# Optimization experiments

Measured on AMD Instinct MI355X. Metric: run time of the kernel, lower is better.

The kernel has to match this reference:

```python
import jax, jax.numpy as jnp
import numpy as np

DIM_Q = 512
DIM_K = 512
DIM_V = 512
NUM_HEADS = 8
B, NQ, NK = 8, 1024, 1024
EPS = 1e-5


def _layer_norm(x, gamma, beta):
    mu = jnp.mean(x, axis=-1, keepdims=True)
    var = jnp.var(x, axis=-1, keepdims=True)
    return (x - mu) * jax.lax.rsqrt(var + EPS) * gamma + beta


def setup_inputs() -> dict:
    key = jax.random.key(0)
    ks = jax.random.split(key, 12)

    def lin(k, fan_in, fan_out):
        bound = 1.0 / np.sqrt(fan_in)
        kw, kb = jax.random.split(k)
        W = jax.random.uniform(kw, (fan_in, fan_out), jnp.float32, -bound, bound)
        b = jax.random.uniform(kb, (fan_out,), jnp.float32, -bound, bound)
        return W, b

    Q = jax.random.normal(ks[0], (B, NQ, DIM_Q), jnp.float32)
    K = jax.random.normal(ks[1], (B, NK, DIM_K), jnp.float32)
    Wq, bq = lin(ks[2], DIM_Q, DIM_V)
    Wk, bk = lin(ks[3], DIM_K, DIM_V)
    Wv, bv = lin(ks[4], DIM_K, DIM_V)
    Wo, bo = lin(ks[5], DIM_V, DIM_V)
    g0 = jnp.ones((DIM_V,), jnp.float32)
    be0 = jnp.zeros((DIM_V,), jnp.float32)
    g1 = jnp.ones((DIM_V,), jnp.float32)
    be1 = jnp.zeros((DIM_V,), jnp.float32)
    return {"Q": Q, "K": K, "Wq": Wq, "bq": bq, "Wk": Wk, "bk": bk,
            "Wv": Wv, "bv": bv, "Wo": Wo, "bo": bo,
            "g0": g0, "be0": be0, "g1": g1, "be1": be1}


def reference(Q, K, Wq, bq, Wk, bk, Wv, bv, Wo, bo, g0, be0, g1, be1):
    H = NUM_HEADS
    d = DIM_V // H
    b, nq, _ = Q.shape
    nk = K.shape[1]

    Qp = (Q @ Wq + bq).reshape(b, nq, H, d)   # [B,Nq,H,d]
    Kp = (K @ Wk + bk).reshape(b, nk, H, d)   # [B,Nk,H,d]
    Vp = (K @ Wv + bv).reshape(b, nk, H, d)   # [B,Nk,H,d]

    # NOTE: original scales by sqrt(dim_V), not sqrt(head_dim)
    scores = jnp.einsum("bqhd,bkhd->bhqk", Qp, Kp) / jnp.sqrt(
        jnp.asarray(DIM_V, Qp.dtype))
    A = jax.nn.softmax(scores, axis=-1)                     # [B,H,Nq,Nk]
    O = Qp + jnp.einsum("bhqk,bkhd->bqhd", A, Vp)           # residual inside heads
    O = O.reshape(b, nq, DIM_V)
    O = _layer_norm(O, g0, be0)
    O = O + jax.nn.relu(O @ Wo + bo)
    O = _layer_norm(O, g1, be1)
    return O
```

## Files before the change

### kernel.cpp

```cpp
#include <hip/hip_runtime.h>
#include <hip/hip_bf16.h>

typedef __attribute__((ext_vector_type(8))) short short8;
typedef __attribute__((ext_vector_type(4))) short s16x4;
typedef __attribute__((ext_vector_type(4))) float f32x4;

#define DIMV 512
#define NHEAD 8
#define NBATCH 8
#define NQL 1024
#define NKL 1024
#define QSCALE (0.04419417382415922f * 1.44269504088896340f)

__device__ __forceinline__ short f2bf(float f) {
    unsigned int u = __float_as_uint(f);
    unsigned int r = (u + 0x7fffu + ((u >> 16) & 1u)) >> 16;
    return (short)r;
}
__device__ __forceinline__ float bf2f(short s) {
    return __uint_as_float(((unsigned int)(unsigned short)s) << 16);
}
__device__ __forceinline__ unsigned cvt_pk_bf16(float a, float b) {
    unsigned r;
    asm("v_cvt_pk_bf16_f32 %0, %1, %2" : "=v"(r) : "v"(a), "v"(b));
    return r;
}
__device__ __forceinline__ short8 pack8(float4 x, float4 y) {
    union { unsigned u[4]; short8 s; } u;
    u.u[0] = cvt_pk_bf16(x.x, x.y); u.u[1] = cvt_pk_bf16(x.z, x.w);
    u.u[2] = cvt_pk_bf16(y.x, y.y); u.u[3] = cvt_pk_bf16(y.z, y.w);
    return u.s;
}
__device__ __forceinline__ void gload16(const void* g, void* l) {
    __builtin_amdgcn_global_load_lds(
        (const __attribute__((address_space(1))) unsigned int*)g,
        (__attribute__((address_space(3))) unsigned int*)l, 16, 0, 0);
}

__global__ void k_transpose_w4(const float* __restrict__ w0, const float* __restrict__ w1,
                               const float* __restrict__ w2, const float* __restrict__ w3,
                               short* __restrict__ t0, short* __restrict__ t1,
                               short* __restrict__ t2, short* __restrict__ t3) {
    __shared__ float tile[32][33];
    const float* W; short* Wt;
    int z = blockIdx.z;
    if (z == 0)      { W = w0; Wt = t0; }
    else if (z == 1) { W = w1; Wt = t1; }
    else if (z == 2) { W = w2; Wt = t2; }
    else             { W = w3; Wt = t3; }
    int tx = threadIdx.x, ty = threadIdx.y;
    int n0 = blockIdx.x * 32, k0 = blockIdx.y * 32;
    #pragma unroll
    for (int r = 0; r < 4; ++r)
        tile[ty + r * 8][tx] = W[(size_t)(k0 + ty + r * 8) * DIMV + n0 + tx];
    __syncthreads();
    #pragma unroll
    for (int r = 0; r < 4; ++r)
        Wt[(size_t)(n0 + ty + r * 8) * DIMV + k0 + tx] = f2bf(tile[tx][ty + r * 8]);
}

#define GLSA 72
__global__ __launch_bounds__(256) void k_gemm_qkv(
    const float* __restrict__ Qf, const float* __restrict__ Kf,
    const short* __restrict__ Wqt, const short* __restrict__ Wkvt,
    const float* __restrict__ bq, const float* __restrict__ bk,
    const float* __restrict__ bv,
    short* __restrict__ Qpb, short* __restrict__ Kp, short* __restrict__ VT)
{
    __shared__ __align__(16) short As[128 * GLSA];
    __shared__ __align__(16) short Bs[64 * GLSA];
    int tid = threadIdx.x;
    int lane = tid & 63, wid = tid >> 6;
    int wr = wid >> 1, wc = wid & 1;
    int c = lane & 15, g = lane >> 4;
    int bid = blockIdx.x;
    bool isQ = bid < 512;
    int lb = isQ ? bid : bid - 512;
    int NBX = isQ ? 8 : 16;
    int xcd = lb & 7, slot = lb >> 3;
    int bx = slot % NBX;
    int by = xcd + 8 * (slot / NBX);
    int m0 = by * 128, n0 = bx * 64;
    const float* Ag0 = isQ ? Qf : Kf;
    const short* Bt = isQ ? Wqt : Wkvt;

    int ar = tid >> 2, kc4 = (tid & 3) * 16;
    const float* Ag = Ag0 + (size_t)(m0 + ar) * 512 + kc4;
    int br = tid >> 3, kc8 = (tid & 7) * 8;
    const short* Bg = Bt + (size_t)(n0 + br) * 512 + kc8;

    f32x4 acc[4][2] = {};
    float4 aA[4], aB[4]; short8 b0, b1;
    #pragma unroll
    for (int i = 0; i < 4; ++i) {
        aA[i] = *reinterpret_cast<const float4*>(Ag + i * 4);
        aB[i] = *reinterpret_cast<const float4*>(Ag + 64 * 512 + i * 4);
    }
    b0 = *reinterpret_cast<const short8*>(Bg);
    b1 = *reinterpret_cast<const short8*>(Bg + 32 * 512);

    for (int k0 = 0; k0 < 512; k0 += 64) {
        *reinterpret_cast<short8*>(&As[ar * GLSA + kc4]) = pack8(aA[0], aA[1]);
        *reinterpret_cast<short8*>(&As[ar * GLSA + kc4 + 8]) = pack8(aA[2], aA[3]);
        *reinterpret_cast<short8*>(&As[(ar + 64) * GLSA + kc4]) = pack8(aB[0], aB[1]);
        *reinterpret_cast<short8*>(&As[(ar + 64) * GLSA + kc4 + 8]) = pack8(aB[2], aB[3]);
        *reinterpret_cast<short8*>(&Bs[br * GLSA + kc8]) = b0;
        *reinterpret_cast<short8*>(&Bs[(br + 32) * GLSA + kc8]) = b1;
        __syncthreads();
        if (k0 < 448) {
            #pragma unroll
            for (int i = 0; i < 4; ++i) {
                aA[i] = *reinterpret_cast<const float4*>(Ag + k0 + 64 + i * 4);
                aB[i] = *reinterpret_cast<const float4*>(Ag + k0 + 64 + 64 * 512 + i * 4);
            }
            b0 = *reinterpret_cast<const short8*>(Bg + k0 + 64);
            b1 = *reinterpret_cast<const short8*>(Bg + k0 + 64 + 32 * 512);
        }
        #pragma unroll
        for (int ks = 0; ks < 2; ++ks) {
            short8 af[4], bf[2];
            #pragma unroll
            for (int i = 0; i < 4; ++i)
                af[i] = *reinterpret_cast<short8*>(&As[(wr * 64 + i * 16 + c) * GLSA + ks * 32 + g * 8]);
            #pragma unroll
            for (int j = 0; j < 2; ++j)
                bf[j] = *reinterpret_cast<short8*>(&Bs[(wc * 32 + j * 16 + c) * GLSA + ks * 32 + g * 8]);
            #pragma unroll
            for (int i = 0; i < 4; ++i)
                #pragma unroll
                for (int j = 0; j < 2; ++j)
                    acc[i][j] = __builtin_amdgcn_mfma_f32_16x16x32_bf16(af[i], bf[j], acc[i][j], 0, 0, 0);
        }
        __syncthreads();
    }

    int vb = m0 >> 10, kvb = m0 & 1023;
    #pragma unroll
    for (int i = 0; i < 4; ++i)
        #pragma unroll
        for (int j = 0; j < 2; ++j) {
            int rrow = wr * 64 + i * 16 + g * 4;
            int row = m0 + rrow;
            int col = n0 + wc * 32 + j * 16 + c;
            if (isQ) {
                float bb = bq[col];
                #pragma unroll
                for (int q = 0; q < 4; ++q)
                    Qpb[(size_t)(row + q) * 512 + col] = f2bf((acc[i][j][q] + bb) * QSCALE);
            } else if (col < 512) {
                float bb = bk[col];
                #pragma unroll
                for (int q = 0; q < 4; ++q)
                    Kp[(size_t)(row + q) * 512 + col] = f2bf(acc[i][j][q] + bb);
            } else {
                int colv = col - 512;
                float bb = bv[colv];
                s16x4 pk;
                #pragma unroll
                for (int q = 0; q < 4; ++q) pk[q] = f2bf(acc[i][j][q] + bb);
                *reinterpret_cast<s16x4*>(
                    &VT[((size_t)(vb * 512 + colv)) * 1024 + kvb + rrow]) = pk;
            }
        }
}

__global__ __launch_bounds__(256) void k_gemm_o(
    const short* __restrict__ A, const short* __restrict__ Bt,
    const float* __restrict__ bias, short* __restrict__ outB,
    const short* __restrict__ residB)
{
    __shared__ __align__(16) short As[128 * GLSA];
    __shared__ __align__(16) short Bs[64 * GLSA];
    int tid = threadIdx.x;
    int lane = tid & 63, wid = tid >> 6;
    int wr = wid >> 1, wc = wid & 1;
    int c = lane & 15, g = lane >> 4;
    int lb = blockIdx.x;
    int xcd = lb & 7, slot = lb >> 3;
    int bx = slot & 7;
    int by = xcd + 8 * (slot >> 3);
    int m0 = by * 128, n0 = bx * 64;

    int ar = tid >> 2, kc4 = (tid & 3) * 16;
    const short* Ag = A + (size_t)(m0 + ar) * 512 + kc4;
    int br = tid >> 3, kc8 = (tid & 7) * 8;
    const short* Bg = Bt + (size_t)(n0 + br) * 512 + kc8;

    f32x4 acc[4][2] = {};
    short8 a0, a1, a2, a3, b0, b1;
    a0 = *reinterpret_cast<const short8*>(Ag);
    a1 = *reinterpret_cast<const short8*>(Ag + 8);
    a2 = *reinterpret_cast<const short8*>(Ag + 64 * 512);
    a3 = *reinterpret_cast<const short8*>(Ag + 64 * 512 + 8);
    b0 = *reinterpret_cast<const short8*>(Bg);
    b1 = *reinterpret_cast<const short8*>(Bg + 32 * 512);

    for (int k0 = 0; k0 < 512; k0 += 64) {
        *reinterpret_cast<short8*>(&As[ar * GLSA + kc4]) = a0;
        *reinterpret_cast<short8*>(&As[ar * GLSA + kc4 + 8]) = a1;
        *reinterpret_cast<short8*>(&As[(ar + 64) * GLSA + kc4]) = a2;
        *reinterpret_cast<short8*>(&As[(ar + 64) * GLSA + kc4 + 8]) = a3;
        *reinterpret_cast<short8*>(&Bs[br * GLSA + kc8]) = b0;
        *reinterpret_cast<short8*>(&Bs[(br + 32) * GLSA + kc8]) = b1;
        __syncthreads();
        if (k0 < 448) {
            a0 = *reinterpret_cast<const short8*>(Ag + k0 + 64);
            a1 = *reinterpret_cast<const short8*>(Ag + k0 + 64 + 8);
            a2 = *reinterpret_cast<const short8*>(Ag + k0 + 64 + 64 * 512);
            a3 = *reinterpret_cast<const short8*>(Ag + k0 + 64 + 64 * 512 + 8);
            b0 = *reinterpret_cast<const short8*>(Bg + k0 + 64);
            b1 = *reinterpret_cast<const short8*>(Bg + k0 + 64 + 32 * 512);
        }
        #pragma unroll
        for (int ks = 0; ks < 2; ++ks) {
            short8 af[4], bf[2];
            #pragma unroll
            for (int i = 0; i < 4; ++i)
                af[i] = *reinterpret_cast<short8*>(&As[(wr * 64 + i * 16 + c) * GLSA + ks * 32 + g * 8]);
            #pragma unroll
            for (int j = 0; j < 2; ++j)
                bf[j] = *reinterpret_cast<short8*>(&Bs[(wc * 32 + j * 16 + c) * GLSA + ks * 32 + g * 8]);
            #pragma unroll
            for (int i = 0; i < 4; ++i)
                #pragma unroll
                for (int j = 0; j < 2; ++j)
                    acc[i][j] = __builtin_amdgcn_mfma_f32_16x16x32_bf16(af[i], bf[j], acc[i][j], 0, 0, 0);
        }
        __syncthreads();
    }

    #pragma unroll
    for (int i = 0; i < 4; ++i)
        #pragma unroll
        for (int j = 0; j < 2; ++j) {
            int row = m0 + wr * 64 + i * 16 + g * 4;
            int col = n0 + wc * 32 + j * 16 + c;
            float bb = bias[col];
            #pragma unroll
            for (int q = 0; q < 4; ++q) {
                size_t idx = (size_t)(row + q) * 512 + col;
                outB[idx] = f2bf(bf2f(residB[idx]) + fmaxf(acc[i][j][q] + bb, 0.f));
            }
        }
}

__global__ __launch_bounds__(512) void k_attn(
    const short* __restrict__ Qb, const short* __restrict__ Kb,
    const short* __restrict__ VTb, const short* __restrict__ RgBase,
    short* __restrict__ Out)
{
    constexpr float RSCALE = 1.0f / QSCALE;
    __shared__ __align__(16) short Ks[2][64 * 64];
    __shared__ __align__(16) short Vt[2][64 * 64];
    __shared__ __align__(16) short Ps[128 * 72];
    int tid = threadIdx.x;
    int lane = tid & 63, w = tid >> 6;
    int c = lane & 15, g = lane >> 4;
    int bid = blockIdx.x;
    int grp = bid & 63, qb = bid >> 6;
    int h = grp & 7, b = grp >> 3;
    const short* Qg = Qb + (size_t)(b * NQL + qb * 128) * 512 + h * 64;
    const short* Kg = Kb + (size_t)b * NKL * 512 + h * 64;
    const short* VTg = VTb + (size_t)(b * 512 + h * 64) * NKL;
    const short* Rg = RgBase + (size_t)(b * NQL + qb * 128) * 512 + h * 64;
    short* Og = Out + (size_t)(b * NQL + qb * 128) * 512 + h * 64;

    short8 qf[2];
    #pragma unroll
    for (int ks = 0; ks < 2; ++ks)
        qf[ks] = *reinterpret_cast<const short8*>(&Qg[(size_t)(w * 16 + c) * 512 + ks * 32 + g * 8]);

    int sr = tid >> 3, ss = tid & 7;
    int sg = ss ^ (sr & 7);
    const short* Kgc = Kg + (size_t)sr * 512 + sg * 8;
    const short* Vgc = VTg + (size_t)sr * 1024 + sg * 8;
    char* KsB = (char*)&Ks[0][0];
    char* VtB = (char*)&Vt[0][0];
    int wbase = (tid & ~63) * 16;

    gload16(Kgc, KsB + wbase);
    gload16(Vgc, VtB + wbase);
    __syncthreads();

    float m = -1e30f, l = 0.f;
    f32x4 o[4] = {};
    int swz = (c & 7) * 8;

    for (int t = 0; t < 16; ++t) {
        int cur = t & 1;
        if (t < 15) {
            int nxt = cur ^ 1;
            gload16(Kgc + (size_t)(t + 1) * 64 * 512, KsB + nxt * 8192 + wbase);
            gload16(Vgc + (t + 1) * 64, VtB + nxt * 8192 + wbase);
        }

        f32x4 s[4] = {};
        #pragma unroll
        for (int ks = 0; ks < 2; ++ks) {
            #pragma unroll
            for (int i = 0; i < 4; ++i) {
                short8 ak = *reinterpret_cast<short8*>(
                    &Ks[cur][(i * 16 + c) * 64 + (((ks * 4 + g) * 8) ^ swz)]);
                s[i] = __builtin_amdgcn_mfma_f32_16x16x32_bf16(ak, qf[ks], s[i], 0, 0, 0);
            }
        }

        float r0 = fmaxf(fmaxf(s[0][0], s[0][1]), fmaxf(s[0][2], s[0][3]));
        float r1 = fmaxf(fmaxf(s[1][0], s[1][1]), fmaxf(s[1][2], s[1][3]));
        float r2 = fmaxf(fmaxf(s[2][0], s[2][1]), fmaxf(s[2][2], s[2][3]));
        float r3 = fmaxf(fmaxf(s[3][0], s[3][1]), fmaxf(s[3][2], s[3][3]));
        float rowm = fmaxf(fmaxf(r0, r1), fmaxf(r2, r3));
        rowm = fmaxf(rowm, __shfl_xor(rowm, 16));
        rowm = fmaxf(rowm, __shfl_xor(rowm, 32));
        if (!__all(rowm <= m + 8.f)) {
            float mnew = fmaxf(m, rowm);
            float corr = __builtin_amdgcn_exp2f(m - mnew);
            l *= corr;
            float cq[4];
            #pragma unroll
            for (int q = 0; q < 4; ++q) cq[q] = __shfl(corr, g * 4 + q);
            #pragma unroll
            for (int jf = 0; jf < 4; ++jf)
                #pragma unroll
                for (int q = 0; q < 4; ++q)
                    o[jf][q] *= cq[q];
            m = mnew;
        }
        float psum = 0.f;
        #pragma unroll
        for (int i = 0; i < 4; ++i) {
            float p0 = __builtin_amdgcn_exp2f(s[i][0] - m);
            float p1 = __builtin_amdgcn_exp2f(s[i][1] - m);
            float p2 = __builtin_amdgcn_exp2f(s[i][2] - m);
            float p3 = __builtin_amdgcn_exp2f(s[i][3] - m);
            psum += (p0 + p1) + (p2 + p3);
            uint2 pw;
            pw.x = cvt_pk_bf16(p0, p1);
            pw.y = cvt_pk_bf16(p2, p3);
            *reinterpret_cast<uint2*>(&Ps[(w * 16 + c) * 72 + i * 16 + g * 4]) = pw;
        }
        psum += __shfl_xor(psum, 16);
        psum += __shfl_xor(psum, 32);
        l += psum;

        #pragma unroll
        for (int ks = 0; ks < 2; ++ks) {
            short8 pa = *reinterpret_cast<short8*>(&Ps[(w * 16 + c) * 72 + ks * 32 + g * 8]);
            #pragma unroll
            for (int jf = 0; jf < 4; ++jf) {
                short8 vb = *reinterpret_cast<short8*>(
                    &Vt[cur][(jf * 16 + c) * 64 + (((ks * 4 + g) * 8) ^ swz)]);
                o[jf] = __builtin_amdgcn_mfma_f32_16x16x32_bf16(pa, vb, o[jf], 0, 0, 0);
            }
        }

        __syncthreads();
    }

    float linv = 1.f / l;
    float lq[4];
    #pragma unroll
    for (int q = 0; q < 4; ++q) lq[q] = __shfl(linv, g * 4 + q);
    #pragma unroll
    for (int jf = 0; jf < 4; ++jf)
        #pragma unroll
        for (int q = 0; q < 4; ++q) {
            int r = w * 16 + g * 4 + q;
            int d = jf * 16 + c;
            size_t idx = (size_t)r * 512 + d;
            Og[idx] = f2bf(o[jf][q] * lq[q] + bf2f(Rg[idx]) * RSCALE);
        }
}

__global__ __launch_bounds__(64) void k_ln(
    const short* __restrict__ inB,
    float* __restrict__ outF, short* __restrict__ outB,
    const float* __restrict__ gamma, const float* __restrict__ beta)
{
    int row = blockIdx.x, lane = threadIdx.x;
    float vals[8];
    short8 v = *reinterpret_cast<const short8*>(&inB[(size_t)row * 512 + lane * 8]);
    #pragma unroll
    for (int j = 0; j < 8; ++j) vals[j] = bf2f(v[j]);
    float sum = 0.f, sq = 0.f;
    #pragma unroll
    for (int j = 0; j < 8; ++j) { sum += vals[j]; sq += vals[j] * vals[j]; }
    #pragma unroll
    for (int mask = 32; mask; mask >>= 1) {
        sum += __shfl_xor(sum, mask);
        sq  += __shfl_xor(sq, mask);
    }
    float mean = sum * (1.f / 512.f);
    float var  = sq * (1.f / 512.f) - mean * mean;
    float rstd = rsqrtf(var + 1e-5f);
    float y[8];
    #pragma unroll
    for (int j = 0; j < 8; ++j) {
        int col = lane * 8 + j;
        y[j] = (vals[j] - mean) * rstd * gamma[col] + beta[col];
    }
    size_t base = (size_t)row * 512 + lane * 8;
    if (outF) {
        float4 o0 = {y[0], y[1], y[2], y[3]};
        float4 o1 = {y[4], y[5], y[6], y[7]};
        *reinterpret_cast<float4*>(&outF[base]) = o0;
        *reinterpret_cast<float4*>(&outF[base + 4]) = o1;
    }
    if (outB) {
        int4 p;
        p.x = cvt_pk_bf16(y[0], y[1]); p.y = cvt_pk_bf16(y[2], y[3]);
        p.z = cvt_pk_bf16(y[4], y[5]); p.w = cvt_pk_bf16(y[6], y[7]);
        *reinterpret_cast<int4*>(&outB[base]) = p;
    }
}

extern "C" void kernel_launch(void* const* d_in, const int* in_sizes, int n_in,
                              void* d_out, int out_size, void* d_ws, size_t ws_size,
                              hipStream_t stream) {
    const float* Q   = (const float*)d_in[0];
    const float* K   = (const float*)d_in[1];
    const float* Wq  = (const float*)d_in[2];
    const float* bq  = (const float*)d_in[3];
    const float* Wk  = (const float*)d_in[4];
    const float* bk  = (const float*)d_in[5];
    const float* Wv  = (const float*)d_in[6];
    const float* bv  = (const float*)d_in[7];
    const float* Wo  = (const float*)d_in[8];
    const float* bo  = (const float*)d_in[9];
    const float* g0  = (const float*)d_in[10];
    const float* be0 = (const float*)d_in[11];
    const float* g1  = (const float*)d_in[12];
    const float* be1 = (const float*)d_in[13];
    float* out = (float*)d_out;
    char* ws = (char*)d_ws;
    const size_t MB = 1024 * 1024;

    short* Oa    = (short*)(ws + 0);
    short* Wqt   = (short*)(ws + 16 * MB);
    short* Wkvt  = (short*)(ws + 16 * MB + 512 * 1024);
    short* Wot   = (short*)(ws + 17 * MB + 512 * 1024);
    short* VT    = (short*)(ws + 18 * MB);
    short* Qpb   = (short*)(ws + 34 * MB);
    short* Kp    = (short*)(ws + 42 * MB);
    short* ln0b  = (short*)(ws + 34 * MB);
    short* out2b = (short*)(ws + 42 * MB);

    dim3 tb(32, 8), tg(16, 16, 4);
    k_transpose_w4<<<tg, tb, 0, stream>>>(Wq, Wk, Wv, Wo,
                                          Wqt, Wkvt, Wkvt + 512 * 512, Wot);

    k_gemm_qkv<<<1536, 256, 0, stream>>>(Q, K, Wqt, Wkvt, bq, bk, bv, Qpb, Kp, VT);

    k_attn<<<NBATCH * NHEAD * (NQL / 128), 512, 0, stream>>>(Qpb, Kp, VT, Qpb, Oa);

    k_ln<<<NBATCH * NQL, 64, 0, stream>>>(Oa, nullptr, ln0b, g0, be0);
    k_gemm_o<<<512, 256, 0, stream>>>(ln0b, Wot, bo, out2b, ln0b);
    k_ln<<<NBATCH * NQL, 64, 0, stream>>>(out2b, out, nullptr, g1, be1);
}
```

Baseline: 96.31 us.

## Pre-convert Q/K to bf16 and double-buffer GEMM tiles via direct global-to-LDS loads

Adds a separate kernel that converts the fp32 Q and K inputs to bf16 up front. Both projection GEMMs now stream A and B tiles straight into a double-buffered, XOR-swizzled LDS layout using global_load_lds, overlapping the next tile's load with the current MFMA work. The aim is to cut register staging, in-loop conversion and LDS bank conflicts. The price is an extra kernel launch plus a full read and write of Q and K, and the loop appears to drop one barrier per iteration, which could race on buffer reuse.

```diff
diff --git a/kernel.cpp b/kernel.cpp
--- a/kernel.cpp
+++ b/kernel.cpp
@@ -25,16 +25,23 @@
     asm("v_cvt_pk_bf16_f32 %0, %1, %2" : "=v"(r) : "v"(a), "v"(b));
     return r;
 }
-__device__ __forceinline__ short8 pack8(float4 x, float4 y) {
-    union { unsigned u[4]; short8 s; } u;
-    u.u[0] = cvt_pk_bf16(x.x, x.y); u.u[1] = cvt_pk_bf16(x.z, x.w);
-    u.u[2] = cvt_pk_bf16(y.x, y.y); u.u[3] = cvt_pk_bf16(y.z, y.w);
-    return u.s;
-}
 __device__ __forceinline__ void gload16(const void* g, void* l) {
     __builtin_amdgcn_global_load_lds(
         (const __attribute__((address_space(1))) unsigned int*)g,
         (__attribute__((address_space(3))) unsigned int*)l, 16, 0, 0);
+}
+
+__global__ void k_cvt2(const float* __restrict__ a, const float* __restrict__ b,
+                       short* __restrict__ oa, short* __restrict__ ob, int n) {
+    const float* src = blockIdx.y ? b : a;
+    short* dst = blockIdx.y ? ob : oa;
+    int i = (blockIdx.x * blockDim.x + threadIdx.x) * 4;
+    if (i < n) {
+        float4 v = *reinterpret_cast<const float4*>(src + i);
+        s16x4 o;
+        o[0] = f2bf(v.x); o[1] = f2bf(v.y); o[2] = f2bf(v.z); o[3] = f2bf(v.w);
+        *reinterpret_cast<s16x4*>(dst + i) = o;
+    }
 }
 
 __global__ void k_transpose_w4(const float* __restrict__ w0, const float* __restrict__ w1,
@@ -59,72 +66,60 @@
         Wt[(size_t)(n0 + ty + r * 8) * DIMV + k0 + tx] = f2bf(tile[tx][ty + r * 8]);
 }
 
-#define GLSA 72
 __global__ __launch_bounds__(256) void k_gemm_qkv(
-    const float* __restrict__ Qf, const float* __restrict__ Kf,
+    const short* __restrict__ Qb, const short* __restrict__ Kb,
     const short* __restrict__ Wqt, const short* __restrict__ Wkvt,
     const float* __restrict__ bq, const float* __restrict__ bk,
     const float* __restrict__ bv,
     short* __restrict__ Qpb, short* __restrict__ Kp, short* __restrict__ VT)
 {
-    __shared__ __align__(16) short As[128 * GLSA];
-    __shared__ __align__(16) short Bs[64 * GLSA];
+    __shared__ __align__(16) short As[2][128 * 64];
+    __shared__ __align__(16) short Bs[2][64 * 64];
     int tid = threadIdx.x;
-    int lane = tid & 63, wid = tid >> 6;
-    int wr = wid >> 1, wc = wid & 1;
+    int lane = tid & 63, wv = tid >> 6;
+    int wr = wv >> 1, wc = wv & 1;
     int c = lane & 15, g = lane >> 4;
     int bid = blockIdx.x;
     bool isQ = bid < 512;
     int lb = isQ ? bid : bid - 512;
     int NBX = isQ ? 8 : 16;
     int xcd = lb & 7, slot = lb >> 3;
-    int bx = slot % NBX;
-    int by = xcd + 8 * (slot / NBX);
+    int bx = slot % NBX, by = xcd + 8 * (slot / NBX);
     int m0 = by * 128, n0 = bx * 64;
-    const float* Ag0 = isQ ? Qf : Kf;
+    const short* Ab = isQ ? Qb : Kb;
     const short* Bt = isQ ? Wqt : Wkvt;
 
-    int ar = tid >> 2, kc4 = (tid & 3) * 16;
-    const float* Ag = Ag0 + (size_t)(m0 + ar) * 512 + kc4;
-    int br = tid >> 3, kc8 = (tid & 7) * 8;
-    const short* Bg = Bt + (size_t)(n0 + br) * 512 + kc8;
+    int lr = lane >> 3, ls = lane & 7;
+    int sg = ls ^ lr;
+    const short* Asrc = Ab + (size_t)(m0 + wv * 32 + lr) * 512 + sg * 8;
+    const short* Bsrc = Bt + (size_t)(n0 + wv * 16 + lr) * 512 + sg * 8;
+
+    #define STAGE_QKV(buf, k0)  do {                                          \
+        _Pragma("unroll")                                                     \
+        for (int L = 0; L < 4; ++L)                                           \
+            gload16(Asrc + (k0) + L * 8 * 512, (char*)&As[buf][(wv*32+L*8)*64]);\
+        _Pragma("unroll")                                                     \
+        for (int L = 0; L < 2; ++L)                                           \
+            gload16(Bsrc + (k0) + L * 8 * 512, (char*)&Bs[buf][(wv*16+L*8)*64]);\
+    } while (0)
+
+    STAGE_QKV(0, 0);
+    __syncthreads();
 
     f32x4 acc[4][2] = {};
-    float4 aA[4], aB[4]; short8 b0, b1;
-    #pragma unroll
-    for (int i = 0; i < 4; ++i) {
-        aA[i] = *reinterpret_cast<const float4*>(Ag + i * 4);
-        aB[i] = *reinterpret_cast<const float4*>(Ag + 64 * 512 + i * 4);
-    }
-    b0 = *reinterpret_cast<const short8*>(Bg);
-    b1 = *reinterpret_cast<const short8*>(Bg + 32 * 512);
-
-    for (int k0 = 0; k0 < 512; k0 += 64) {
-        *reinterpret_cast<short8*>(&As[ar * GLSA + kc4]) = pack8(aA[0], aA[1]);
-        *reinterpret_cast<short8*>(&As[ar * GLSA + kc4 + 8]) = pack8(aA[2], aA[3]);
-        *reinterpret_cast<short8*>(&As[(ar + 64) * GLSA + kc4]) = pack8(aB[0], aB[1]);
-        *reinterpret_cast<short8*>(&As[(ar + 64) * GLSA + kc4 + 8]) = pack8(aB[2], aB[3]);
-        *reinterpret_cast<short8*>(&Bs[br * GLSA + kc8]) = b0;
-        *reinterpret_cast<short8*>(&Bs[(br + 32) * GLSA + kc8]) = b1;
-        __syncthreads();
-        if (k0 < 448) {
-            #pragma unroll
-            for (int i = 0; i < 4; ++i) {
-                aA[i] = *reinterpret_cast<const float4*>(Ag + k0 + 64 + i * 4);
-                aB[i] = *reinterpret_cast<const float4*>(Ag + k0 + 64 + 64 * 512 + i * 4);
-            }
-            b0 = *reinterpret_cast<const short8*>(Bg + k0 + 64);
-            b1 = *reinterpret_cast<const short8*>(Bg + k0 + 64 + 32 * 512);
-        }
+    for (int t = 0; t < 8; ++t) {
+        int cur = t & 1;
+        if (t < 7) STAGE_QKV(cur ^ 1, (t + 1) * 64);
         #pragma unroll
         for (int ks = 0; ks < 2; ++ks) {
+            int sl = ((ks * 4 + g) ^ (c & 7)) * 8;
             short8 af[4], bf[2];
             #pragma unroll
             for (int i = 0; i < 4; ++i)
-                af[i] = *reinterpret_cast<short8*>(&As[(wr * 64 + i * 16 + c) * GLSA + ks * 32 + g * 8]);
+                af[i] = *reinterpret_cast<short8*>(&As[cur][(wr * 64 + i * 16 + c) * 64 + sl]);
             #pragma unroll
             for (int j = 0; j < 2; ++j)
-                bf[j] = *reinterpret_cast<short8*>(&Bs[(wc * 32 + j * 16 + c) * GLSA + ks * 32 + g * 8]);
+                bf[j] = *reinterpret_cast<short8*>(&Bs[cur][(wc * 32 + j * 16 + c) * 64 + sl]);
             #pragma unroll
             for (int i = 0; i < 4; ++i)
                 #pragma unroll
@@ -169,57 +164,39 @@
     const float* __restrict__ bias, short* __restrict__ outB,
     const short* __restrict__ residB)
 {
-    __shared__ __align__(16) short As[128 * GLSA];
-    __shared__ __align__(16) short Bs[64 * GLSA];
+    __shared__ __align__(16) short As[2][128 * 64];
+    __shared__ __align__(16) short Bs[2][64 * 64];
     int tid = threadIdx.x;
-    int lane = tid & 63, wid = tid >> 6;
-    int wr = wid >> 1, wc = wid & 1;
+    int lane = tid & 63, wv = tid >> 6;
+    int wr = wv >> 1, wc = wv & 1;
     int c = lane & 15, g = lane >> 4;
     int lb = blockIdx.x;
     int xcd = lb & 7, slot = lb >> 3;
-    int bx = slot & 7;
-    int by = xcd + 8 * (slot >> 3);
+    int bx = slot & 7, by = xcd + 8 * (slot >> 3);
     int m0 = by * 128, n0 = bx * 64;
 
-    int ar = tid >> 2, kc4 = (tid & 3) * 16;
-    const short* Ag = A + (size_t)(m0 + ar) * 512 + kc4;
-    int br = tid >> 3, kc8 = (tid & 7) * 8;
-    const short* Bg = Bt + (size_t)(n0 + br) * 512 + kc8;
+    int lr = lane >> 3, ls = lane & 7;
+    int sg = ls ^ lr;
+    const short* Asrc = A + (size_t)(m0 + wv * 32 + lr) * 512 + sg * 8;
+    const short* Bsrc = Bt + (size_t)(n0 + wv * 16 + lr) * 512 + sg * 8;
+
+    STAGE_QKV(0, 0);
+    __syncthreads();
 
     f32x4 acc[4][2] = {};
-    short8 a0, a1, a2, a3, b0, b1;
-    a0 = *reinterpret_cast<const short8*>(Ag);
-    a1 = *reinterpret_cast<const short8*>(Ag + 8);
-    a2 = *reinterpret_cast<const short8*>(Ag + 64 * 512);
-    a3 = *reinterpret_cast<const short8*>(Ag + 64 * 512 + 8);
-    b0 = *reinterpret_cast<const short8*>(Bg);
-    b1 = *reinterpret_cast<const short8*>(Bg + 32 * 512);
-
-    for (int k0 = 0; k0 < 512; k0 += 64) {
-        *reinterpret_cast<short8*>(&As[ar * GLSA + kc4]) = a0;
-        *reinterpret_cast<short8*>(&As[ar * GLSA + kc4 + 8]) = a1;
-        *reinterpret_cast<short8*>(&As[(ar + 64) * GLSA + kc4]) = a2;
-        *reinterpret_cast<short8*>(&As[(ar + 64) * GLSA + kc4 + 8]) = a3;
-        *reinterpret_cast<short8*>(&Bs[br * GLSA + kc8]) = b0;
-        *reinterpret_cast<short8*>(&Bs[(br + 32) * GLSA + kc8]) = b1;
-        __syncthreads();
-        if (k0 < 448) {
-            a0 = *reinterpret_cast<const short8*>(Ag + k0 + 64);
-            a1 = *reinterpret_cast<const short8*>(Ag + k0 + 64 + 8);
-            a2 = *reinterpret_cast<const short8*>(Ag + k0 + 64 + 64 * 512);
-            a3 = *reinterpret_cast<const short8*>(Ag + k0 + 64 + 64 * 512 + 8);
-            b0 = *reinterpret_cast<const short8*>(Bg + k0 + 64);
-            b1 = *reinterpret_cast<const short8*>(Bg + k0 + 64 + 32 * 512);
-        }
+    for (int t = 0; t < 8; ++t) {
+        int cur = t & 1;
+        if (t < 7) STAGE_QKV(cur ^ 1, (t + 1) * 64);
         #pragma unroll
         for (int ks = 0; ks < 2; ++ks) {
+            int sl = ((ks * 4 + g) ^ (c & 7)) * 8;
             short8 af[4], bf[2];
             #pragma unroll
             for (int i = 0; i < 4; ++i)
-                af[i] = *reinterpret_cast<short8*>(&As[(wr * 64 + i * 16 + c) * GLSA + ks * 32 + g * 8]);
+                af[i] = *reinterpret_cast<short8*>(&As[cur][(wr * 64 + i * 16 + c) * 64 + sl]);
             #pragma unroll
             for (int j = 0; j < 2; ++j)
-                bf[j] = *reinterpret_cast<short8*>(&Bs[(wc * 32 + j * 16 + c) * GLSA + ks * 32 + g * 8]);
+                bf[j] = *reinterpret_cast<short8*>(&Bs[cur][(wc * 32 + j * 16 + c) * 64 + sl]);
             #pragma unroll
             for (int i = 0; i < 4; ++i)
                 #pragma unroll
@@ -435,21 +412,26 @@
     char* ws = (char*)d_ws;
     const size_t MB = 1024 * 1024;
 
-    short* Oa    = (short*)(ws + 0);
+    short* Qb    = (short*)(ws + 0);
+    short* Kb    = (short*)(ws + 8 * MB);
     short* Wqt   = (short*)(ws + 16 * MB);
     short* Wkvt  = (short*)(ws + 16 * MB + 512 * 1024);
     short* Wot   = (short*)(ws + 17 * MB + 512 * 1024);
     short* VT    = (short*)(ws + 18 * MB);
     short* Qpb   = (short*)(ws + 34 * MB);
     short* Kp    = (short*)(ws + 42 * MB);
+    short* Oa    = (short*)(ws + 0);
     short* ln0b  = (short*)(ws + 34 * MB);
     short* out2b = (short*)(ws + 42 * MB);
 
+    int n = NBATCH * NQL * DIMV;
+    dim3 cg(n / 4 / 256, 2);
+    k_cvt2<<<cg, 256, 0, stream>>>(Q, K, Qb, Kb, n);
     dim3 tb(32, 8), tg(16, 16, 4);
     k_transpose_w4<<<tg, tb, 0, stream>>>(Wq, Wk, Wv, Wo,
                                           Wqt, Wkvt, Wkvt + 512 * 512, Wot);
 
-    k_gemm_qkv<<<1536, 256, 0, stream>>>(Q, K, Wqt, Wkvt, bq, bk, bv, Qpb, Kp, VT);
+    k_gemm_qkv<<<1536, 256, 0, stream>>>(Qb, Kb, Wqt, Wkvt, bq, bk, bv, Qpb, Kp, VT);
 
     k_attn<<<NBATCH * NHEAD * (NQL / 128), 512, 0, stream>>>(Qpb, Kp, VT, Qpb, Oa);
 
```

New measurement: 94.01 us. 1.02x faster.
